# Optimization experiments

Measured on AMD Instinct MI355X. Metric: run time of the kernel, lower is better.

Reference implementation:

```python
import jax, jax.numpy as jnp
import numpy as np

HIDDEN = 1024
EMB = HIDDEN // 2          # embedding_dim = hidden_dim // 2
NUM_OPS = 8
BATCH = 16384


def setup_inputs() -> dict:
    key = jax.random.key(0)
    ks = jax.random.split(key, 8)
    x = jax.random.normal(ks[0], (BATCH, HIDDEN), dtype=jnp.float32)
    sampled_ops = jax.random.randint(ks[1], (BATCH,), 0, NUM_OPS, dtype=jnp.int32)
    op_emb = jax.random.normal(ks[2], (NUM_OPS, EMB), dtype=jnp.float32) * 0.02
    # per-expert 2-layer MLP params (Linear stored as [in, out] for x @ W)
    s1 = 1.0 / np.sqrt(HIDDEN + EMB)
    s2 = 1.0 / np.sqrt(HIDDEN)
    W1 = jax.random.uniform(ks[3], (NUM_OPS, HIDDEN + EMB, HIDDEN), jnp.float32, -s1, s1)
    b1 = jax.random.uniform(ks[4], (NUM_OPS, HIDDEN), jnp.float32, -s1, s1)
    W2 = jax.random.uniform(ks[5], (NUM_OPS, HIDDEN, HIDDEN), jnp.float32, -s2, s2)
    b2 = jax.random.uniform(ks[6], (NUM_OPS, HIDDEN), jnp.float32, -s2, s2)
    return {"x": x, "sampled_ops": sampled_ops, "op_emb": op_emb,
            "W1": W1, "b1": b1, "W2": W2, "b2": b2}


def reference(x, sampled_ops, op_emb, W1, b1, W2, b2):
    # gather per-token operator embedding and augment input
    emb = jnp.take(op_emb, sampled_ops, axis=0)            # [B, EMB]
    x_aug = jnp.concatenate([x, emb], axis=-1)             # [B, H+EMB]
    num_ops = W1.shape[0]
    out = jnp.zeros_like(x)
    # loop over the small fixed expert set; mask-combine per token
    for o in range(num_ops):
        h = jax.nn.relu(x_aug @ W1[o] + b1[o])             # [B, H]
        y = jax.nn.relu(h @ W2[o] + b2[o])                 # [B, H]
        mask = (sampled_ops == o)[:, None]
        out = out + jnp.where(mask, y, 0.0)
    return out
```

## Files before the change

kernel.cpp:

```cpp
#include <hip/hip_runtime.h>
#include <hip/hip_bf16.h>

#define BATCH 16384
#define HID   1024
#define EMBD  512
#define NOPS  8
#define MAXT  136
#define CNTS  16

typedef __attribute__((ext_vector_type(8))) short bf16x8;
typedef __attribute__((ext_vector_type(4))) float f32x4;

__device__ __forceinline__ unsigned short f2bf(float f) {
  unsigned int u = __float_as_uint(f);
  u += 0x7FFF + ((u >> 16) & 1);
  return (unsigned short)(u >> 16);
}

__device__ __forceinline__ unsigned int pk2(float a, float b) {
  __hip_bfloat162 t = __float22bfloat162_rn(make_float2(a, b));
  return *(unsigned int*)(&t);
}

__device__ __forceinline__ void lds_load16(void* lds, const void* g) {
  __builtin_amdgcn_global_load_lds(
      (const __attribute__((address_space(1))) unsigned int*)g,
      (__attribute__((address_space(3))) unsigned int*)lds, 16, 0, 0);
}

__device__ __forceinline__ void decode_bid(int bid, int& g, int& nx) {
  g = 17 * (bid & 7) + (bid >> 6);
  nx = (bid >> 3) & 7;
}

__device__ __forceinline__ void w_prep_tile(const float* __restrict__ W,
                                            short* __restrict__ Wp,
                                            int ks, int nx, int tid) {
  int n = tid & 127, kh = tid >> 7;
  const float* src = W + (size_t)(ks * 32 + kh * 16) * 1024 + nx * 128 + n;
  float v[16];
#pragma unroll
  for (int kk = 0; kk < 16; ++kk) v[kk] = src[(size_t)kk * 1024];
  uint4 a, b;
  a.x = pk2(v[0], v[1]);  a.y = pk2(v[2], v[3]);
  a.z = pk2(v[4], v[5]);  a.w = pk2(v[6], v[7]);
  b.x = pk2(v[8], v[9]);  b.y = pk2(v[10], v[11]);
  b.z = pk2(v[12], v[13]); b.w = pk2(v[14], v[15]);
  uint4* dst = (uint4*)(Wp + (size_t)n * 32);
  dst[kh * 2] = a;
  dst[kh * 2 + 1] = b;
}

__global__ void bucket_w1_k(const int* __restrict__ ops, int* __restrict__ cnt,
                            int* __restrict__ idx, const float* __restrict__ W1,
                            short* __restrict__ W1p, const float* __restrict__ emb,
                            const float* __restrict__ b1, float* __restrict__ ce) {
  int bid = blockIdx.x;
  int tid = threadIdx.x;
  if (bid >= 64 && bid < 64 + 2048) {
    int b = bid - 64;
    int e = b / 256; int r = b % 256; int nx = r / 32, ks = r % 32;
    w_prep_tile(W1 + (size_t)e * 1536 * 1024,
                W1p + ((size_t)(e * 8 + nx) * 32 + ks) * 4096, ks, nx, tid);
    return;
  }
  if (bid >= 64 + 2048) {
    __shared__ float se[EMBD];
    int b2 = bid - 64 - 2048;
    int e = b2 >> 2, part = b2 & 3;
    int n = part * 256 + tid;
    se[tid] = emb[e * EMBD + tid];
    se[tid + 256] = emb[e * EMBD + tid + 256];
    __syncthreads();
    const float* Wc = W1 + (size_t)e * 1536 * 1024 + (size_t)1024 * 1024 + n;
    float acc = b1[e * HID + n];
#pragma unroll 8
    for (int k = 0; k < EMBD; ++k) acc += se[k] * Wc[(size_t)k * 1024];
    ce[e * HID + n] = acc;
    return;
  }
  __shared__ int wcnt[4][NOPS];
  __shared__ int wbase[4][NOPS];
  int lane = tid & 63, w = tid >> 6;
  int t = bid * 256 + tid;
  int op = ops[t];
  unsigned long long msave = 0;
#pragma unroll
  for (int o = 0; o < NOPS; ++o) {
    unsigned long long mm = __ballot(op == o);
    if (op == o) msave = mm;
    if (lane == o) wcnt[w][o] = __popcll(mm);
  }
  __syncthreads();
  if (tid < NOPS) {
    int c0 = wcnt[0][tid], c1 = wcnt[1][tid], c2 = wcnt[2][tid], c3 = wcnt[3][tid];
    int base = atomicAdd(&cnt[tid * CNTS], c0 + c1 + c2 + c3);
    wbase[0][tid] = base;
    wbase[1][tid] = base + c0;
    wbase[2][tid] = base + c0 + c1;
    wbase[3][tid] = base + c0 + c1 + c2;
  }
  __syncthreads();
  int pre = __popcll(msave & ((1ull << lane) - 1ull));
  idx[op * BATCH + wbase[w][op] + pre] = t;
}

__global__ void schedule_k(const int* __restrict__ cnt, int* __restrict__ desc,
                           int* __restrict__ ntp, int* __restrict__ idx) {
  if (threadIdx.x == 0) {
    int n = 0;
    for (int e = 0; e < NOPS; ++e) {
      int c = cnt[e * CNTS];
      for (int t = 0; t < c; t += 128) { desc[2 * n] = e; desc[2 * n + 1] = t; ++n; }
    }
    *ntp = n;
  }
  for (int e = 0; e < NOPS; ++e) {
    int c = cnt[e * CNTS];
    int cp = (c + 127) & ~127;
    for (int p = c + (int)threadIdx.x; p < cp; p += 256) idx[e * BATCH + p] = 0;
  }
}

__global__ void prep_a_k(const float* __restrict__ x,
                         const int* __restrict__ idx, const int* __restrict__ desc,
                         const int* __restrict__ ntp, short* __restrict__ Ap) {
  __shared__ int toks[128];
  int bid = blockIdx.x;
  int g = bid >> 3, kx = bid & 7;
  if (g >= *ntp) return;
  int e = desc[2 * g], rs = desc[2 * g + 1];
  int tid = threadIdx.x;
  if (tid < 128) toks[tid] = idx[e * BATCH + rs + tid];
  __syncthreads();
  int r = tid >> 1, ah = tid & 1;
  int tok = toks[r];
  short* dst0 = Ap + (size_t)g * 32 * 4096;
#pragma unroll
  for (int kk = 0; kk < 4; ++kk) {
    int ks = kx * 4 + kk;
    const float* src = x + (size_t)tok * HID + ks * 32 + ah * 16;
    float4 f0 = ((const float4*)src)[0];
    float4 f1 = ((const float4*)src)[1];
    float4 f2v = ((const float4*)src)[2];
    float4 f3 = ((const float4*)src)[3];
    uint4 p0 = make_uint4(pk2(f0.x, f0.y), pk2(f0.z, f0.w), pk2(f1.x, f1.y), pk2(f1.z, f1.w));
    uint4 p1 = make_uint4(pk2(f2v.x, f2v.y), pk2(f2v.z, f2v.w), pk2(f3.x, f3.y), pk2(f3.z, f3.w));
    short* dst = dst0 + ks * 4096 + r * 32 + ah * 16;
    ((uint4*)dst)[0] = p0;
    ((uint4*)dst)[1] = p1;
  }
}

__global__ __launch_bounds__(256) void gemm1_w2_k(
    const short* __restrict__ Ap, const float* __restrict__ ce,
    const short* __restrict__ W1p, unsigned short* __restrict__ hp,
    const int* __restrict__ desc, const int* __restrict__ ntp,
    const float* __restrict__ W2, short* __restrict__ W2p) {
  int bid = blockIdx.x;
  int tid = threadIdx.x;
  if (bid >= 8 * MAXT) {
    int b = bid - 8 * MAXT;
    int e = b / 256; int r = b % 256; int nx = r / 32, ks = r % 32;
    w_prep_tile(W2 + (size_t)e * 1024 * 1024,
                W2p + ((size_t)(e * 8 + nx) * 32 + ks) * 4096, ks, nx, tid);
    return;
  }
  int g, nx;
  decode_bid(bid, g, nx);
  if (g >= *ntp) return;
  int e = desc[2 * g];

  __shared__ __align__(16) char smem[16384];
  short* lA = (short*)smem;
  short* lB = (short*)(smem + 8192);

  int lane = tid & 63, w = tid >> 6;
  int wm = w >> 1, wn = w & 1;
  int fr = lane & 15, fq = lane >> 4;

  const char* Asrc = (const char*)Ap + (size_t)g * 32 * 8192;
  const char* Bsrc = (const char*)W1p + (size_t)(e * 8 + nx) * 32 * 8192;

  f32x4 acc[4][4] = {};

  for (int ks = 0; ks < 32; ++ks) {
    const char* as = Asrc + ks * 8192;
    const char* bs = Bsrc + ks * 8192;
    lds_load16(smem + w * 1024, as + w * 1024 + lane * 16);
    lds_load16(smem + 4096 + w * 1024, as + 4096 + w * 1024 + lane * 16);
    lds_load16(smem + 8192 + w * 1024, bs + w * 1024 + lane * 16);
    lds_load16(smem + 12288 + w * 1024, bs + 4096 + w * 1024 + lane * 16);
    __syncthreads();

    bf16x8 af[4], bfr[4];
#pragma unroll
    for (int i = 0; i < 4; ++i)
      af[i] = *(const bf16x8*)&lA[(wm * 64 + i * 16 + fr) * 32 + fq * 8];
#pragma unroll
    for (int j = 0; j < 4; ++j)
      bfr[j] = *(const bf16x8*)&lB[(wn * 64 + j * 16 + fr) * 32 + fq * 8];
#pragma unroll
    for (int i = 0; i < 4; ++i)
#pragma unroll
      for (int j = 0; j < 4; ++j)
        acc[i][j] = __builtin_amdgcn_mfma_f32_16x16x32_bf16(af[i], bfr[j], acc[i][j], 0, 0, 0);
    __syncthreads();
  }

  float bias[4];
#pragma unroll
  for (int j = 0; j < 4; ++j)
    bias[j] = ce[e * HID + nx * 128 + wn * 64 + j * 16 + fr];

  unsigned short* ls = (unsigned short*)smem;
  int lr = lane >> 2;
#pragma unroll
  for (int i = 0; i < 4; ++i) {
    __syncthreads();
#pragma unroll
    for (int j = 0; j < 4; ++j)
#pragma unroll
      for (int rg = 0; rg < 4; ++rg) {
        float v = acc[i][j][rg] + bias[j];
        v = v > 0.f ? v : 0.f;
        ls[w * 1024 + (fq * 4 + rg) * 64 + j * 16 + fr] = f2bf(v);
      }
    __syncthreads();
    int R = wm * 64 + i * 16 + lr;
#pragma unroll
    for (int s = 0; s < 2; ++s) {
      int ch = (lane & 3) + s * 4;
      int ks2 = nx * 4 + wn * 2 + (ch >> 2);
      uint4 val = *(const uint4*)&ls[w * 1024 + lr * 64 + ch * 8];
      *(uint4*)(hp + ((size_t)(g * 32 + ks2) * 128 + R) * 32 + (ch & 3) * 8) = val;
    }
  }
}

__global__ __launch_bounds__(256) void gemm2_k(
    const unsigned short* __restrict__ hp, const float* __restrict__ b2,
    const short* __restrict__ W2p, float* __restrict__ out,
    const int* __restrict__ idx, const int* __restrict__ cnt,
    const int* __restrict__ desc, const int* __restrict__ ntp) {
  int g, nx;
  decode_bid(blockIdx.x, g, nx);
  if (g >= *ntp) return;
  int e = desc[2 * g], rs = desc[2 * g + 1];
  int ce2 = cnt[e * CNTS];

  __shared__ __align__(16) char smem[16384];
  __shared__ int toks[128];
  short* lA = (short*)smem;
  short* lB = (short*)(smem + 8192);

  int tid = threadIdx.x, lane = tid & 63, w = tid >> 6;
  int wm = w >> 1, wn = w & 1;
  int fr = lane & 15, fq = lane >> 4;

  if (tid < 128) toks[tid] = idx[e * BATCH + rs + tid];

  const char* Asrc = (const char*)hp + (size_t)g * 32 * 8192;
  const char* Bsrc = (const char*)W2p + (size_t)(e * 8 + nx) * 32 * 8192;

  f32x4 acc[4][4] = {};

  for (int ks = 0; ks < 32; ++ks) {
    const char* as = Asrc + ks * 8192;
    const char* bs = Bsrc + ks * 8192;
    lds_load16(smem + w * 1024, as + w * 1024 + lane * 16);
    lds_load16(smem + 4096 + w * 1024, as + 4096 + w * 1024 + lane * 16);
    lds_load16(smem + 8192 + w * 1024, bs + w * 1024 + lane * 16);
    lds_load16(smem + 12288 + w * 1024, bs + 4096 + w * 1024 + lane * 16);
    __syncthreads();

    bf16x8 af[4], bfr[4];
#pragma unroll
    for (int i = 0; i < 4; ++i)
      af[i] = *(const bf16x8*)&lA[(wm * 64 + i * 16 + fr) * 32 + fq * 8];
#pragma unroll
    for (int j = 0; j < 4; ++j)
      bfr[j] = *(const bf16x8*)&lB[(wn * 64 + j * 16 + fr) * 32 + fq * 8];
#pragma unroll
    for (int i = 0; i < 4; ++i)
#pragma unroll
      for (int j = 0; j < 4; ++j)
        acc[i][j] = __builtin_amdgcn_mfma_f32_16x16x32_bf16(af[i], bfr[j], acc[i][j], 0, 0, 0);
    __syncthreads();
  }

  float bias[4];
#pragma unroll
  for (int j = 0; j < 4; ++j)
    bias[j] = b2[e * HID + nx * 128 + wn * 64 + j * 16 + fr];

  float* lsf = (float*)smem;
  int lr = lane >> 2;
#pragma unroll
  for (int i = 0; i < 4; ++i) {
    __syncthreads();
#pragma unroll
    for (int j = 0; j < 4; ++j)
#pragma unroll
      for (int rg = 0; rg < 4; ++rg) {
        float v = acc[i][j][rg] + bias[j];
        lsf[w * 1024 + (fq * 4 + rg) * 64 + j * 16 + fr] = v > 0.f ? v : 0.f;
      }
    __syncthreads();
    int R = wm * 64 + i * 16 + lr;
    if (R < ce2 - rs) {
      float* orow = out + (size_t)toks[R] * HID + nx * 128 + wn * 64;
#pragma unroll
      for (int s = 0; s < 4; ++s) {
        int ch = (lane & 3) + s * 4;
        *(float4*)(orow + ch * 4) = *(const float4*)&lsf[w * 1024 + lr * 64 + ch * 4];
      }
    }
  }
}


extern "C" void kernel_launch(void* const* d_in, const int* in_sizes, int n_in,
                              void* d_out, int out_size, void* d_ws, size_t ws_size,
                              hipStream_t stream) {
  const float* x   = (const float*)d_in[0];
  const int*   ops = (const int*)d_in[1];
  const float* emb = (const float*)d_in[2];
  const float* W1  = (const float*)d_in[3];
  const float* b1  = (const float*)d_in[4];
  const float* W2  = (const float*)d_in[5];
  const float* b2  = (const float*)d_in[6];
  float* out = (float*)d_out;

  char* ws = (char*)d_ws;
  int* cnt  = (int*)(ws + 0);
  int* ntp  = (int*)(ws + 1024);
  int* desc = (int*)(ws + 1280);
  int* idx  = (int*)(ws + 4096);
  short* W1p = (short*)(ws + 528384);
  short* W2p = (short*)(ws + 17305600);
  float* ce  = (float*)(ws + 34082816);
  unsigned short* hp = (unsigned short*)(ws + 34115584);
  short* Ap = (short*)(ws + 69767168);

  hipMemsetAsync(cnt, 0, 512, stream);
  bucket_w1_k<<<64 + 2048 + 32, 256, 0, stream>>>(ops, cnt, idx, W1, W1p, emb, b1, ce);
  schedule_k<<<1, 256, 0, stream>>>(cnt, desc, ntp, idx);
  prep_a_k<<<8 * MAXT, 256, 0, stream>>>(x, idx, desc, ntp, Ap);
  gemm1_w2_k<<<8 * MAXT + 2048, 256, 0, stream>>>(Ap, ce, W1p, hp, desc, ntp, W2, W2p);
  gemm2_k<<<8 * MAXT, 256, 0, stream>>>(hp, b2, W2p, out, idx, cnt, desc, ntp);
}
```

Baseline: 340.0 us.

## Split-K embedding bias with atomics and move W1 repack into prep kernel

Rewrites the per-expert embedding contribution (emb @ W1_emb + b1) as a 16-way split-K computation. Each block reads float4 rows of W1 and combines partials with atomicAdd into a zeroed ce buffer, replacing 32 serial long-loop blocks. The W1 bf16 repack tiles move out of the bucketing kernel and into the activation prep kernel, so bucketing finishes quickly and the repack overlaps with the gather of x. The cost is extra float atomics and a larger memset, and the atomic ordering makes ce summation order nondeterministic.

```diff
diff --git a/kernel.cpp b/kernel.cpp
--- a/kernel.cpp
+++ b/kernel.cpp
@@ -51,38 +51,37 @@
   dst[kh * 2 + 1] = b;
 }
 
-__global__ void bucket_w1_k(const int* __restrict__ ops, int* __restrict__ cnt,
+__global__ void bucket_ce_k(const int* __restrict__ ops, int* __restrict__ cnt,
                             int* __restrict__ idx, const float* __restrict__ W1,
-                            short* __restrict__ W1p, const float* __restrict__ emb,
+                            const float* __restrict__ emb,
                             const float* __restrict__ b1, float* __restrict__ ce) {
   int bid = blockIdx.x;
   int tid = threadIdx.x;
-  if (bid >= 64 && bid < 64 + 2048) {
-    int b = bid - 64;
-    int e = b / 256; int r = b % 256; int nx = r / 32, ks = r % 32;
-    w_prep_tile(W1 + (size_t)e * 1536 * 1024,
-                W1p + ((size_t)(e * 8 + nx) * 32 + ks) * 4096, ks, nx, tid);
-    return;
-  }
-  if (bid >= 64 + 2048) {
-    __shared__ float se[EMBD];
-    int b2 = bid - 64 - 2048;
-    int e = b2 >> 2, part = b2 & 3;
-    int n = part * 256 + tid;
-    se[tid] = emb[e * EMBD + tid];
-    se[tid + 256] = emb[e * EMBD + tid + 256];
-    __syncthreads();
-    const float* Wc = W1 + (size_t)e * 1536 * 1024 + (size_t)1024 * 1024 + n;
-    float acc = b1[e * HID + n];
-#pragma unroll 8
-    for (int k = 0; k < EMBD; ++k) acc += se[k] * Wc[(size_t)k * 1024];
-    ce[e * HID + n] = acc;
+  if (bid < 128) {
+    int e = bid >> 4, kp = bid & 15;
+    int n = tid * 4;
+    const float* Wc = W1 + (size_t)e * 1536 * 1024 + (size_t)(1024 + kp * 32) * 1024 + n;
+    const float* ee = emb + e * EMBD + kp * 32;
+    float4 a = make_float4(0.f, 0.f, 0.f, 0.f);
+#pragma unroll
+    for (int kk = 0; kk < 32; ++kk) {
+      float s = ee[kk];
+      float4 r = *(const float4*)(Wc + (size_t)kk * 1024);
+      a.x += s * r.x; a.y += s * r.y; a.z += s * r.z; a.w += s * r.w;
+    }
+    if (kp == 0) {
+      float4 b = *(const float4*)(b1 + e * HID + n);
+      a.x += b.x; a.y += b.y; a.z += b.z; a.w += b.w;
+    }
+    float* d = ce + e * HID + n;
+    atomicAdd(d + 0, a.x); atomicAdd(d + 1, a.y);
+    atomicAdd(d + 2, a.z); atomicAdd(d + 3, a.w);
     return;
   }
   __shared__ int wcnt[4][NOPS];
   __shared__ int wbase[4][NOPS];
   int lane = tid & 63, w = tid >> 6;
-  int t = bid * 256 + tid;
+  int t = (bid - 128) * 256 + tid;
   int op = ops[t];
   unsigned long long msave = 0;
 #pragma unroll
@@ -122,15 +121,23 @@
   }
 }
 
-__global__ void prep_a_k(const float* __restrict__ x,
-                         const int* __restrict__ idx, const int* __restrict__ desc,
-                         const int* __restrict__ ntp, short* __restrict__ Ap) {
+__global__ void prep_k(const float* __restrict__ x,
+                       const int* __restrict__ idx, const int* __restrict__ desc,
+                       const int* __restrict__ ntp, short* __restrict__ Ap,
+                       const float* __restrict__ W1, short* __restrict__ W1p) {
+  int bid = blockIdx.x;
+  int tid = threadIdx.x;
+  if (bid >= 8 * MAXT) {
+    int b = bid - 8 * MAXT;
+    int e = b / 256; int r = b % 256; int nx = r / 32, ks = r % 32;
+    w_prep_tile(W1 + (size_t)e * 1536 * 1024,
+                W1p + ((size_t)(e * 8 + nx) * 32 + ks) * 4096, ks, nx, tid);
+    return;
+  }
   __shared__ int toks[128];
-  int bid = blockIdx.x;
   int g = bid >> 3, kx = bid & 7;
   if (g >= *ntp) return;
   int e = desc[2 * g], rs = desc[2 * g + 1];
-  int tid = threadIdx.x;
   if (tid < 128) toks[tid] = idx[e * BATCH + rs + tid];
   __syncthreads();
   int r = tid >> 1, ah = tid & 1;
@@ -334,19 +341,19 @@
 
   char* ws = (char*)d_ws;
   int* cnt  = (int*)(ws + 0);
-  int* ntp  = (int*)(ws + 1024);
-  int* desc = (int*)(ws + 1280);
-  int* idx  = (int*)(ws + 4096);
-  short* W1p = (short*)(ws + 528384);
-  short* W2p = (short*)(ws + 17305600);
-  float* ce  = (float*)(ws + 34082816);
+  float* ce = (float*)(ws + 512);
+  int* ntp  = (int*)(ws + 33280);
+  int* desc = (int*)(ws + 33344);
+  int* idx  = (int*)(ws + 36864);
+  short* W1p = (short*)(ws + 561152);
+  short* W2p = (short*)(ws + 17338368);
   unsigned short* hp = (unsigned short*)(ws + 34115584);
   short* Ap = (short*)(ws + 69767168);
 
-  hipMemsetAsync(cnt, 0, 512, stream);
-  bucket_w1_k<<<64 + 2048 + 32, 256, 0, stream>>>(ops, cnt, idx, W1, W1p, emb, b1, ce);
+  hipMemsetAsync(ws, 0, 33280, stream);
+  bucket_ce_k<<<128 + 64, 256, 0, stream>>>(ops, cnt, idx, W1, emb, b1, ce);
   schedule_k<<<1, 256, 0, stream>>>(cnt, desc, ntp, idx);
-  prep_a_k<<<8 * MAXT, 256, 0, stream>>>(x, idx, desc, ntp, Ap);
+  prep_k<<<8 * MAXT + 2048, 256, 0, stream>>>(x, idx, desc, ntp, Ap, W1, W1p);
   gemm1_w2_k<<<8 * MAXT + 2048, 256, 0, stream>>>(Ap, ce, W1p, hp, desc, ntp, W2, W2p);
   gemm2_k<<<8 * MAXT, 256, 0, stream>>>(hp, b2, W2p, out, idx, cnt, desc, ntp);
 }
```

After: 303.4 us. -10.8%, faster.
